# Performance work log

Measured on AMD Instinct MI355X. Metric: run time of the kernel, lower is better.

Reference implementation:

```python
import jax, jax.numpy as jnp
import numpy as np

B, S, DIM = 2, 2048, 768
HEADS, HEAD_DIM = 12, 64
WINDOW = 512
LEVELS, EXP = 4, 4
LR = 0.1
LN_EPS = 1e-5


def layernorm(x, g, b):
    m = jnp.mean(x, axis=-1, keepdims=True)
    v = jnp.mean(jnp.square(x - m), axis=-1, keepdims=True)
    return (x - m) * jax.lax.rsqrt(v + LN_EPS) * g + b


def setup_inputs() -> dict:
    key = jax.random.key(0)
    ks = jax.random.split(key, 12)
    D = DIM
    w = lambda k, shape: jax.random.normal(k, shape, jnp.float32) * 0.02
    return {
        "x": jax.random.normal(ks[0], (B, S, D), jnp.float32),
        # nn.MultiheadAttention params (packed qkv in_proj + out_proj)
        "in_proj_w": w(ks[1], (3 * D, D)),
        "in_proj_b": jnp.zeros((3 * D,), jnp.float32),
        "out_proj_w": w(ks[2], (D, D)),
        "out_proj_b": jnp.zeros((D,), jnp.float32),
        "ln_local_g": jnp.ones((D,), jnp.float32),
        "ln_local_b": jnp.zeros((D,), jnp.float32),
        # SelfModifyingTitans (delta-rule linear memory) params
        "t_wq": w(ks[3], (HEADS * HEAD_DIM, D)),
        "t_wk": w(ks[4], (HEADS * HEAD_DIM, D)),
        "t_wv": w(ks[5], (HEADS * HEAD_DIM, D)),
        "t_wo": w(ks[6], (D, HEADS * HEAD_DIM)),
        "ln_tit_g": jnp.ones((D,), jnp.float32),
        "ln_tit_b": jnp.zeros((D,), jnp.float32),
        # combine gate
        "gate_w": w(ks[7], (D, 2 * D)),
        "gate_b": jnp.zeros((D,), jnp.float32),
        # ContinuumMemorySystem: LEVELS stacked FFNs dim -> EXP*dim -> dim
        "cms_w1": w(ks[8], (LEVELS, EXP * D, D)),
        "cms_b1": jnp.zeros((LEVELS, EXP * D), jnp.float32),
        "cms_w2": w(ks[9], (LEVELS, D, EXP * D)),
        "cms_b2": jnp.zeros((LEVELS, D), jnp.float32),
        "ln_cms_g": jnp.ones((D,), jnp.float32),
        "ln_cms_b": jnp.zeros((D,), jnp.float32),
    }


def reference(x, in_proj_w, in_proj_b, out_proj_w, out_proj_b, ln_local_g,
              ln_local_b, t_wq, t_wk, t_wv, t_wo, ln_tit_g, ln_tit_b,
              gate_w, gate_b, cms_w1, cms_b1, cms_w2, cms_b2,
              ln_cms_g, ln_cms_b):
    Bq, Sq, D = x.shape
    H, dh = HEADS, D // HEADS

    # ---- causal sliding-window MHA (mask True = blocked in torch; here keep allowed) ----
    i = jnp.arange(Sq)[:, None]
    j = jnp.arange(Sq)[None, :]
    allowed = (j <= i) & (j > i - WINDOW)  # [S, S]

    qkv = x @ in_proj_w.T + in_proj_b  # [B,S,3D]
    q, k, v = jnp.split(qkv, 3, axis=-1)
    split_heads = lambda t: t.reshape(Bq, Sq, H, dh).transpose(0, 2, 1, 3)
    q, k, v = split_heads(q), split_heads(k), split_heads(v)
    scale = 1.0 / np.sqrt(dh).astype(np.float32)
    scores = jnp.einsum('bhqd,bhkd->bhqk', q * scale, k)
    scores = jnp.where(allowed, scores, jnp.finfo(scores.dtype).min)
    attn = jax.nn.softmax(scores, axis=-1)
    o = jnp.einsum('bhqk,bhkd->bhqd', attn, v)
    local_out = o.transpose(0, 2, 1, 3).reshape(Bq, Sq, D) @ out_proj_w.T + out_proj_b
    x_local = layernorm(x + local_out, ln_local_g, ln_local_b)

    # ---- SelfModifyingTitans: delta-rule recurrent associative memory ----
    tq = (x @ t_wq.T).reshape(Bq, Sq, HEADS, HEAD_DIM).transpose(1, 0, 2, 3)  # [S,B,H,dh]
    tk = (x @ t_wk.T).reshape(Bq, Sq, HEADS, HEAD_DIM).transpose(1, 0, 2, 3)
    tv = (x @ t_wv.T).reshape(Bq, Sq, HEADS, HEAD_DIM).transpose(1, 0, 2, 3)

    def step(M, qkv_t):
        qt, kt, vt = qkv_t  # each [B,H,dh]
        pred = jnp.einsum('bhde,bhd->bhe', M, kt)
        M = M + LR * jnp.einsum('bhd,bhe->bhde', kt, vt - pred)  # delta rule
        ot = jnp.einsum('bhde,bhd->bhe', M, qt)
        return M, ot

    M0 = jnp.zeros((Bq, HEADS, HEAD_DIM, HEAD_DIM), x.dtype)
    memory_state, os_seq = jax.lax.scan(step, M0, (tq, tk, tv))
    titans_out = os_seq.transpose(1, 0, 2, 3).reshape(Bq, Sq, HEADS * HEAD_DIM) @ t_wo.T
    x_global = layernorm(x + titans_out, ln_tit_g, ln_tit_b)

    # ---- gated combine ----
    gate = jax.nn.sigmoid(jnp.concatenate([x_local, x_global], axis=-1) @ gate_w.T + gate_b)
    xc = gate * x_local + (1.0 - gate) * x_global

    # ---- ContinuumMemorySystem: average of LEVELS FFNs ----
    h = jnp.einsum('bsd,lfd->blsf', xc, cms_w1) + cms_b1[None, :, None, :]
    h = jax.nn.gelu(h)
    cms = jnp.einsum('blsf,ldf->blsd', h, cms_w2) + cms_b2[None, :, None, :]
    cms_out = cms.mean(axis=1)

    out = layernorm(xc + cms_out, ln_cms_g, ln_cms_b)
    return out, memory_state
```

## Files before the change

### kernel.cpp

```cpp
#include <hip/hip_runtime.h>
#include <hip/hip_bf16.h>
#include <math.h>

typedef unsigned short u16;
typedef __attribute__((ext_vector_type(8))) short bf8v;
typedef __attribute__((ext_vector_type(4))) short bf4v;
typedef __attribute__((ext_vector_type(4))) float f4v;

__device__ __forceinline__ float bf2f(u16 h) {
    unsigned int u = ((unsigned int)h) << 16;
    float f;
    __builtin_memcpy(&f, &u, 4);
    return f;
}
__device__ __forceinline__ u16 f2bf(float f) {
    unsigned int u;
    __builtin_memcpy(&u, &f, 4);
    unsigned int r = (u + 0x7FFFu + ((u >> 16) & 1u)) >> 16;
    return (u16)r;
}
__device__ __forceinline__ float gelu_tanh(float x) {
    float x3 = x * x * x;
    float y = 0.7978845608028654f * (x + 0.044715f * x3);
    float e = __expf(2.f * y);
    float t = 1.f - 2.f / (e + 1.f);
    return 0.5f * x * (1.f + t);
}

#define SEQ 2048
#define DIMC 768
#define NHEAD 12
#define QKVC 2304
#define LRc 0.1f

__global__ __launch_bounds__(256) void cast_f2b_kernel(
    const float* __restrict__ src, u16* __restrict__ dst, int n)
{
    int i = (blockIdx.x * 256 + threadIdx.x) * 4;
    if (i + 3 < n) {
        float4 v = *(const float4*)(src + i);
        dst[i + 0] = f2bf(v.x);
        dst[i + 1] = f2bf(v.y);
        dst[i + 2] = f2bf(v.z);
        dst[i + 3] = f2bf(v.w);
    }
}

__global__ __launch_bounds__(256) void cast2_f2b_kernel(
    const float* __restrict__ s0, u16* __restrict__ d0,
    const float* __restrict__ s1, u16* __restrict__ d1, int n)
{
    const float* s = blockIdx.z ? s1 : s0;
    u16* d = blockIdx.z ? d1 : d0;
    int i = (blockIdx.x * 256 + threadIdx.x) * 4;
    if (i + 3 < n) {
        float4 v = *(const float4*)(s + i);
        d[i + 0] = f2bf(v.x);
        d[i + 1] = f2bf(v.y);
        d[i + 2] = f2bf(v.z);
        d[i + 3] = f2bf(v.w);
    }
}

__global__ __launch_bounds__(256) void cast_split_kernel(
    const float* __restrict__ src, u16* __restrict__ hi, u16* __restrict__ lo, int n)
{
    int i = (blockIdx.x * 256 + threadIdx.x) * 4;
    if (i + 3 < n) {
        float4 v = *(const float4*)(src + i);
        float vv[4] = {v.x, v.y, v.z, v.w};
        #pragma unroll
        for (int j = 0; j < 4; ++j) {
            u16 h = f2bf(vv[j]);
            hi[i + j] = h;
            lo[i + j] = f2bf(vv[j] - bf2f(h));
        }
    }
}

__device__ __forceinline__ void gemm128_body(
    const u16* __restrict__ A, const u16* __restrict__ W,
    const float* __restrict__ bias, u16* __restrict__ outb, float* __restrict__ outf,
    int N, int Kloop, int Kstride, int act, int mode, float oscale)
{
    __shared__ u16 As[128 * 32];
    __shared__ u16 Bs[128 * 32];
    const int tid  = threadIdx.x;
    const int lane = tid & 63;
    const int wv   = tid >> 6;
    const int r16  = lane & 15;
    const int quad = lane >> 4;
    const int mh   = (wv & 1) * 64;
    const int nh   = (wv >> 1) * 64;
    const int m_blk = blockIdx.x * 128;
    const int n_blk = blockIdx.y * 128;

    const int c0 = tid, c1 = tid + 256;
    const u16* Ag0 = A + (size_t)(m_blk + (c0 >> 2)) * Kstride + (c0 & 3) * 8;
    const u16* Ag1 = A + (size_t)(m_blk + (c1 >> 2)) * Kstride + (c1 & 3) * 8;
    const u16* Wg0 = W + (size_t)(n_blk + (c0 >> 2)) * Kstride + (c0 & 3) * 8;
    const u16* Wg1 = W + (size_t)(n_blk + (c1 >> 2)) * Kstride + (c1 & 3) * 8;
    u16* As0 = As + c0 * 8;
    u16* As1 = As + c1 * 8;
    u16* Bs0 = Bs + c0 * 8;
    u16* Bs1 = Bs + c1 * 8;

    f4v acc[4][4];
    #pragma unroll
    for (int i = 0; i < 4; ++i)
        #pragma unroll
        for (int j = 0; j < 4; ++j) acc[i][j] = (f4v){0.f, 0.f, 0.f, 0.f};

    bf8v av0 = *(const bf8v*)Ag0;
    bf8v av1 = *(const bf8v*)Ag1;
    bf8v bv0 = *(const bf8v*)Wg0;
    bf8v bv1 = *(const bf8v*)Wg1;
    for (int k0 = 0; k0 < Kloop; k0 += 32) {
        __syncthreads();
        *(bf8v*)As0 = av0;
        *(bf8v*)As1 = av1;
        *(bf8v*)Bs0 = bv0;
        *(bf8v*)Bs1 = bv1;
        __syncthreads();
        if (k0 + 32 < Kloop) {
            av0 = *(const bf8v*)(Ag0 + k0 + 32);
            av1 = *(const bf8v*)(Ag1 + k0 + 32);
            bv0 = *(const bf8v*)(Wg0 + k0 + 32);
            bv1 = *(const bf8v*)(Wg1 + k0 + 32);
        }
        bf8v af[4], bfj[4];
        #pragma unroll
        for (int i = 0; i < 4; ++i)
            af[i] = *(const bf8v*)(As + (mh + i * 16 + r16) * 32 + quad * 8);
        #pragma unroll
        for (int j = 0; j < 4; ++j)
            bfj[j] = *(const bf8v*)(Bs + (nh + j * 16 + r16) * 32 + quad * 8);
        #pragma unroll
        for (int i = 0; i < 4; ++i)
            #pragma unroll
            for (int j = 0; j < 4; ++j)
                acc[i][j] = __builtin_amdgcn_mfma_f32_16x16x32_bf16(af[i], bfj[j], acc[i][j], 0, 0, 0);
    }

    #pragma unroll
    for (int j = 0; j < 4; ++j) {
        int gn = n_blk + nh + j * 16 + r16;
        float bvv = bias ? bias[gn] : 0.f;
        #pragma unroll
        for (int i = 0; i < 4; ++i) {
            #pragma unroll
            for (int rr = 0; rr < 4; ++rr) {
                int gm = m_blk + mh + i * 16 + quad * 4 + rr;
                float v = acc[i][j][rr] + bvv;
                if (act == 1) v = gelu_tanh(v);
                else if (act == 2) v = 1.f / (1.f + __expf(-v));
                size_t oi = (size_t)gm * N + gn;
                if (mode == 0) outb[oi] = f2bf(v);
                else if (mode == 1) outf[oi] = oscale * v;
                else if (mode == 2) outf[oi] += oscale * v;
                else atomicAdd(outf + oi, oscale * v);
            }
        }
    }
}

__global__ __launch_bounds__(256) void gemm128_kernel(
    const u16* __restrict__ A, const u16* __restrict__ W,
    const float* __restrict__ bias, u16* __restrict__ outb, float* __restrict__ outf,
    int N, int K, int act, int mode, float oscale)
{
    gemm128_body(A, W, bias, outb, outf, N, K, K, act, mode, oscale);
}

__global__ __launch_bounds__(256) void gemm128_dual_kernel(
    const u16* __restrict__ A0, const u16* __restrict__ W0,
    const float* __restrict__ b0, u16* __restrict__ o0,
    const u16* __restrict__ A1, const u16* __restrict__ W1,
    const float* __restrict__ b1, u16* __restrict__ o1,
    int N, int K)
{
    if (blockIdx.z == 0) gemm128_body(A0, W0, b0, o0, nullptr, N, K, K, 0, 0, 0.f);
    else                 gemm128_body(A1, W1, b1, o1, nullptr, N, K, K, 0, 0, 0.f);
}

__global__ __launch_bounds__(256) void gemm128_ksplit_kernel(
    const u16* __restrict__ A, const u16* __restrict__ W,
    const float* __restrict__ bias, float* __restrict__ outf,
    int N, int Kstride, int KC, float oscale)
{
    const int z = blockIdx.z;
    gemm128_body(A + (size_t)z * KC, W + (size_t)z * KC, z == 0 ? bias : nullptr,
                 nullptr, outf, N, KC, Kstride, 0, 3, oscale);
}

__global__ __launch_bounds__(256) void gemm_split_kernel(
    const u16* __restrict__ Ahi, const u16* __restrict__ Alo,
    const u16* __restrict__ W0hi, const u16* __restrict__ W0lo, float* __restrict__ out0,
    const u16* __restrict__ W1hi, const u16* __restrict__ W1lo, float* __restrict__ out1,
    int M, int N, int K)
{
    const u16* Whi = blockIdx.z ? W1hi : W0hi;
    const u16* Wlo = blockIdx.z ? W1lo : W0lo;
    float* outf    = blockIdx.z ? out1 : out0;

    const int lane = threadIdx.x & 63;
    const int wv   = threadIdx.x >> 6;
    const int m0   = blockIdx.x * 64 + wv * 16;
    const int n0   = blockIdx.y * 64;
    const int r16  = lane & 15;
    const int quad = lane >> 4;

    const size_t arow = (size_t)(m0 + r16) * K + quad * 8;
    const size_t wrow = (size_t)(n0 + r16) * K + quad * 8;
    const size_t wstride = (size_t)16 * K;

    f4v acc[4];
    #pragma unroll
    for (int j = 0; j < 4; ++j) acc[j] = (f4v){0.f, 0.f, 0.f, 0.f};

    for (int k0 = 0; k0 < K; k0 += 32) {
        bf8v ah = *(const bf8v*)(Ahi + arow + k0);
        bf8v al = *(const bf8v*)(Alo + arow + k0);
        #pragma unroll
        for (int j = 0; j < 4; ++j) {
            bf8v bh = *(const bf8v*)(Whi + wrow + j * wstride + k0);
            bf8v bl = *(const bf8v*)(Wlo + wrow + j * wstride + k0);
            acc[j] = __builtin_amdgcn_mfma_f32_16x16x32_bf16(ah, bh, acc[j], 0, 0, 0);
            acc[j] = __builtin_amdgcn_mfma_f32_16x16x32_bf16(ah, bl, acc[j], 0, 0, 0);
            acc[j] = __builtin_amdgcn_mfma_f32_16x16x32_bf16(al, bh, acc[j], 0, 0, 0);
        }
    }

    #pragma unroll
    for (int j = 0; j < 4; ++j) {
        int gn = n0 + j * 16 + r16;
        #pragma unroll
        for (int rr = 0; rr < 4; ++rr) {
            int gm = m0 + quad * 4 + rr;
            outf[(size_t)gm * N + gn] = acc[j][rr];
        }
    }
}

#define NJ 527
#define NJP 548
__global__ __launch_bounds__(256) void attn_kernel(
    const u16* __restrict__ qkv, u16* __restrict__ outp)
{
    const int bh = blockIdx.y;
    const int b = bh / NHEAD, h = bh % NHEAD;
    const int q0 = blockIdx.x * 16;
    const int jbase = q0 - 511;
    const int tid = threadIdx.x;
    const int lane = tid & 63;
    const int wv = tid >> 6;
    const int r16 = lane & 15;
    const int quad = lane >> 4;

    __shared__ float ss[16][NJP];
    __shared__ float redbuf[16][17];
    __shared__ float rowmax[16];
    __shared__ float rowinv[16];

    const size_t qrow = (size_t)(b * SEQ + q0 + r16) * QKVC + h * 64 + quad * 8;
    bf8v qf0 = *(const bf8v*)(qkv + qrow);
    bf8v qf1 = *(const bf8v*)(qkv + qrow + 32);

    for (int jt = wv; jt < 33; jt += 4) {
        int js_l = jt * 16 + r16;
        int j = jbase + js_l;
        int jc = j & (SEQ - 1);
        const u16* kp = qkv + (size_t)(b * SEQ + jc) * QKVC + DIMC + h * 64 + quad * 8;
        bf8v kf0 = *(const bf8v*)kp;
        bf8v kf1 = *(const bf8v*)(kp + 32);
        f4v acc = (f4v){0.f, 0.f, 0.f, 0.f};
        acc = __builtin_amdgcn_mfma_f32_16x16x32_bf16(qf0, kf0, acc, 0, 0, 0);
        acc = __builtin_amdgcn_mfma_f32_16x16x32_bf16(qf1, kf1, acc, 0, 0, 0);
        if (js_l < NJ) {
            #pragma unroll
            for (int rr = 0; rr < 4; ++rr) {
                int row = quad * 4 + rr;
                bool ok = (j >= 0) && (js_l >= row) && (js_l <= row + 511);
                ss[row][js_l] = ok ? 0.125f * acc[rr] : -1e30f;
            }
        }
    }
    for (int t = tid; t < 16 * 17; t += 256)
        ss[t / 17][527 + t % 17] = 0.f;
    __syncthreads();

    {
        int r = tid >> 4, l16 = tid & 15;
        float mx = -1e30f;
        #pragma unroll 1
        for (int js = l16; js < NJ; js += 16) mx = fmaxf(mx, ss[r][js]);
        redbuf[r][l16] = mx;
        __syncthreads();
        if (l16 == 0) {
            float m = -1e30f;
            #pragma unroll
            for (int i = 0; i < 16; ++i) m = fmaxf(m, redbuf[r][i]);
            rowmax[r] = m;
        }
        __syncthreads();
        float rm = rowmax[r];
        float sm = 0.f;
        #pragma unroll 1
        for (int js = l16; js < NJ; js += 16) {
            float p = __expf(ss[r][js] - rm);
            ss[r][js] = p;
            sm += p;
        }
        redbuf[r][l16] = sm;
        __syncthreads();
        if (l16 == 0) {
            float s = 0.f;
            #pragma unroll
            for (int i = 0; i < 16; ++i) s += redbuf[r][i];
            rowinv[r] = 1.f / s;
        }
        __syncthreads();
    }

    {
        const int d0 = wv * 16;
        const u16* vp = qkv + (size_t)b * SEQ * QKVC + 2 * DIMC + h * 64 + d0 + r16;
        f4v oacc = (f4v){0.f, 0.f, 0.f, 0.f};
        for (int k0 = 0; k0 < 544; k0 += 32) {
            float4 p0 = *(const float4*)&ss[r16][k0 + quad * 8];
            float4 p1 = *(const float4*)&ss[r16][k0 + quad * 8 + 4];
            bf8v pa;
            pa[0] = (short)f2bf(p0.x); pa[1] = (short)f2bf(p0.y);
            pa[2] = (short)f2bf(p0.z); pa[3] = (short)f2bf(p0.w);
            pa[4] = (short)f2bf(p1.x); pa[5] = (short)f2bf(p1.y);
            pa[6] = (short)f2bf(p1.z); pa[7] = (short)f2bf(p1.w);
            bf8v vb;
            #pragma unroll
            for (int m = 0; m < 8; ++m) {
                int j = jbase + k0 + quad * 8 + m;
                int jc = j & (SEQ - 1);
                vb[m] = (short)vp[(size_t)jc * QKVC];
            }
            oacc = __builtin_amdgcn_mfma_f32_16x16x32_bf16(pa, vb, oacc, 0, 0, 0);
        }
        #pragma unroll
        for (int rr = 0; rr < 4; ++rr) {
            int row = quad * 4 + rr;
            size_t oi = (size_t)(b * SEQ + q0 + row) * DIMC + h * 64 + d0 + r16;
            outp[oi] = f2bf(oacc[rr] * rowinv[row]);
        }
    }
}

__global__ __launch_bounds__(256) void ln_res_kernel(
    const void* __restrict__ xv, int xf32, const void* __restrict__ yv, int yf32,
    const float* __restrict__ g, const float* __restrict__ be,
    u16* __restrict__ outb, float* __restrict__ outf, int ldout)
{
    const int row = blockIdx.x;
    const int t = threadIdx.x;
    const size_t base = (size_t)row * DIMC;
    float vv[3];
    float s = 0.f, s2 = 0.f;
    #pragma unroll
    for (int i = 0; i < 3; ++i) {
        int d = t + i * 256;
        float a = xf32 ? ((const float*)xv)[base + d] : bf2f(((const u16*)xv)[base + d]);
        float y = yf32 ? ((const float*)yv)[base + d] : bf2f(((const u16*)yv)[base + d]);
        float w = a + y;
        vv[i] = w;
        s += w;
        s2 += w * w;
    }
    #pragma unroll
    for (int o = 32; o > 0; o >>= 1) {
        s  += __shfl_down(s, o);
        s2 += __shfl_down(s2, o);
    }
    __shared__ float rs[4], rq[4], mb[2];
    if ((t & 63) == 0) { rs[t >> 6] = s; rq[t >> 6] = s2; }
    __syncthreads();
    if (t == 0) {
        float S1 = rs[0] + rs[1] + rs[2] + rs[3];
        float S2 = rq[0] + rq[1] + rq[2] + rq[3];
        float mean = S1 * (1.f / 768.f);
        float var = S2 * (1.f / 768.f) - mean * mean;
        mb[0] = mean;
        mb[1] = rsqrtf(var + 1e-5f);
    }
    __syncthreads();
    float mean = mb[0], rstd = mb[1];
    #pragma unroll
    for (int i = 0; i < 3; ++i) {
        int d = t + i * 256;
        float v = (vv[i] - mean) * rstd * g[d] + be[d];
        if (outb) outb[(size_t)row * ldout + d] = f2bf(v);
        else      outf[(size_t)row * ldout + d] = v;
    }
}

__global__ __launch_bounds__(256) void ln_res2_kernel(
    const float* __restrict__ x,
    const u16* __restrict__ y0, const float* __restrict__ g0, const float* __restrict__ b0,
    u16* __restrict__ o0,
    const u16* __restrict__ y1, const float* __restrict__ g1, const float* __restrict__ b1,
    u16* __restrict__ o1, int M)
{
    int row = blockIdx.x;
    const u16* y; const float* g; const float* be; u16* ob;
    if (row < M) { y = y0; g = g0; be = b0; ob = o0; }
    else { row -= M; y = y1; g = g1; be = b1; ob = o1; }
    const int t = threadIdx.x;
    const size_t base = (size_t)row * DIMC;
    float vv[3];
    float s = 0.f, s2 = 0.f;
    #pragma unroll
    for (int i = 0; i < 3; ++i) {
        int d = t + i * 256;
        float w = x[base + d] + bf2f(y[base + d]);
        vv[i] = w;
        s += w;
        s2 += w * w;
    }
    #pragma unroll
    for (int o = 32; o > 0; o >>= 1) {
        s  += __shfl_down(s, o);
        s2 += __shfl_down(s2, o);
    }
    __shared__ float rs[4], rq[4], mb[2];
    if ((t & 63) == 0) { rs[t >> 6] = s; rq[t >> 6] = s2; }
    __syncthreads();
    if (t == 0) {
        float S1 = rs[0] + rs[1] + rs[2] + rs[3];
        float S2 = rq[0] + rq[1] + rq[2] + rq[3];
        float mean = S1 * (1.f / 768.f);
        float var = S2 * (1.f / 768.f) - mean * mean;
        mb[0] = mean;
        mb[1] = rsqrtf(var + 1e-5f);
    }
    __syncthreads();
    float mean = mb[0], rstd = mb[1];
    #pragma unroll
    for (int i = 0; i < 3; ++i) {
        int d = t + i * 256;
        float v = (vv[i] - mean) * rstd * g[d] + be[d];
        ob[(size_t)row * 1536 + d] = f2bf(v);
    }
}

__global__ __launch_bounds__(64) void scanA_kernel(
    const u16* __restrict__ tq, const float* __restrict__ tk,
    float* __restrict__ Tm, float* __restrict__ Sm)
{
    const int bid = blockIdx.x;
    const int bh = bid >> 5, c = bid & 31;
    const int b = bh / NHEAD, h = bh % NHEAD;
    const int lane = threadIdx.x;

    __shared__ float Ks[64][68];
    __shared__ float As[64][68];
    __shared__ float Ts[64][68];
    __shared__ u16   Qs[64][72];

    const size_t rowb = (size_t)b * SEQ * DIMC + h * 64;
    const int rg = lane >> 4, c4 = (lane & 15) * 4;
    #pragma unroll 4
    for (int i = 0; i < 16; ++i) {
        int row = i * 4 + rg;
        size_t g = rowb + (size_t)(c * 64 + row) * DIMC + c4;
        *(float4*)&Ks[row][c4] = *(const float4*)(tk + g);
        *(bf4v*)&Qs[row][c4]   = *(const bf4v*)(tq + g);
    }
    __syncthreads();

    float4 kr4[16];
    #pragma unroll
    for (int d4 = 0; d4 < 16; ++d4) kr4[d4] = *(float4*)&Ks[lane][d4 * 4];

    for (int t = 0; t < 64; ++t) {
        float a = 0.f;
        #pragma unroll
        for (int d4 = 0; d4 < 16; ++d4) {
            float4 kt = *(float4*)&Ks[t][d4 * 4];
            a += kt.x * kr4[d4].x + kt.y * kr4[d4].y + kt.z * kr4[d4].z + kt.w * kr4[d4].w;
        }
        As[t][lane] = (lane < t) ? LRc * a : 0.f;
    }
    Ts[0][lane] = (lane == 0) ? 1.f : 0.f;
    for (int t = 1; t < 64; ++t) {
        float s = (lane == t) ? 1.f : 0.f;
        for (int tau = 0; tau < t; ++tau)
            s -= As[t][tau] * Ts[tau][lane];
        Ts[t][lane] = s;
    }
    for (int t = 0; t < 64; ++t) {
        float a = 0.f;
        #pragma unroll
        for (int d4 = 0; d4 < 16; ++d4) {
            bf4v qt = *(bf4v*)&Qs[t][d4 * 4];
            a += bf2f((u16)qt[0]) * kr4[d4].x + bf2f((u16)qt[1]) * kr4[d4].y
               + bf2f((u16)qt[2]) * kr4[d4].z + bf2f((u16)qt[3]) * kr4[d4].w;
        }
        As[t][lane] = (lane <= t) ? a : 0.f;
    }
    __syncthreads();
    float* Tg = Tm + (size_t)bid * 4096;
    float* Sg = Sm + (size_t)bid * 4096;
    #pragma unroll 4
    for (int i = 0; i < 16; ++i) {
        int row = i * 4 + rg;
        *(float4*)(Tg + row * 64 + c4) = *(float4*)&Ts[row][c4];
        *(float4*)(Sg + row * 64 + c4) = *(float4*)&As[row][c4];
    }
}

__global__ __launch_bounds__(256) void scanB_kernel(
    const u16* __restrict__ tq, const float* __restrict__ tk, const float* __restrict__ tv,
    const float* __restrict__ Tm, const float* __restrict__ Sm,
    u16* __restrict__ tito, float* __restrict__ mout)
{
    const int bid = blockIdx.x;
    const int bh = bid >> 2, eh = bid & 3;
    const int b = bh / NHEAD, h = bh % NHEAD;
    const int tid = threadIdx.x;
    const int tx = tid & 3;
    const int r  = tid >> 2;
    const int cc4 = tx * 4;
    const int e0 = eh * 16;

    __shared__ float Ms[64][20];
    __shared__ float Ys[64][20];
    __shared__ float Us[64][20];
    __shared__ float XK[64][68];
    __shared__ float XT[64][68];
    __shared__ float XS[64][68];
    __shared__ u16   Qt[64][72];

    const size_t rowb = (size_t)b * SEQ * DIMC + h * 64;

    for (int i = tid; i < 64 * 20; i += 256) (&Ms[0][0])[i] = 0.f;

    const int srow = tid & 63;
    const int scc  = (tid >> 6) * 16;

    for (int ch = 0; ch < 32; ++ch) {
        const size_t crow = rowb + (size_t)ch * 64 * DIMC;
        {
            const float* s = tk + crow + (size_t)srow * DIMC + scc;
            float4 a0 = *(const float4*)(s + 0), a1 = *(const float4*)(s + 4),
                   a2 = *(const float4*)(s + 8), a3 = *(const float4*)(s + 12);
            float av[16] = {a0.x, a0.y, a0.z, a0.w, a1.x, a1.y, a1.z, a1.w,
                            a2.x, a2.y, a2.z, a2.w, a3.x, a3.y, a3.z, a3.w};
            #pragma unroll
            for (int j = 0; j < 16; ++j) XK[scc + j][srow] = av[j];
            const u16* qg = tq + crow + (size_t)srow * DIMC + scc;
            bf8v q0 = *(const bf8v*)(qg), q1 = *(const bf8v*)(qg + 8);
            #pragma unroll
            for (int j = 0; j < 8; ++j) {
                Qt[scc + j][srow]     = (u16)q0[j];
                Qt[scc + 8 + j][srow] = (u16)q1[j];
            }
        }
        __syncthreads();

        const float* tsrc = Tm + ((size_t)(bh * 32 + ch)) * 4096 + (size_t)srow * 64 + scc;
        float4 t0 = *(const float4*)(tsrc + 0), t1 = *(const float4*)(tsrc + 4),
               t2 = *(const float4*)(tsrc + 8), t3 = *(const float4*)(tsrc + 12);
        float4 v0 = *(const float4*)(tv + crow + (size_t)r * DIMC + e0 + cc4);

        float p[4] = {0.f, 0.f, 0.f, 0.f};
        float oa[4] = {0.f, 0.f, 0.f, 0.f};
        #pragma unroll 4
        for (int k = 0; k < 64; ++k) {
            float a = XK[k][r];
            float q = bf2f(Qt[k][r]);
            float4 m = *(float4*)&Ms[k][cc4];
            p[0] += a * m.x; p[1] += a * m.y; p[2] += a * m.z; p[3] += a * m.w;
            oa[0] += q * m.x; oa[1] += q * m.y; oa[2] += q * m.z; oa[3] += q * m.w;
        }
        {
            float av[16] = {t0.x, t0.y, t0.z, t0.w, t1.x, t1.y, t1.z, t1.w,
                            t2.x, t2.y, t2.z, t2.w, t3.x, t3.y, t3.z, t3.w};
            #pragma unroll
            for (int j = 0; j < 16; ++j) XT[scc + j][srow] = av[j];
            Ys[r][cc4 + 0] = LRc * (v0.x - p[0]);
            Ys[r][cc4 + 1] = LRc * (v0.y - p[1]);
            Ys[r][cc4 + 2] = LRc * (v0.z - p[2]);
            Ys[r][cc4 + 3] = LRc * (v0.w - p[3]);
        }
        __syncthreads();

        const float* ssrc = Sm + ((size_t)(bh * 32 + ch)) * 4096 + (size_t)srow * 64 + scc;
        float4 s0 = *(const float4*)(ssrc + 0), s1 = *(const float4*)(ssrc + 4),
               s2 = *(const float4*)(ssrc + 8), s3 = *(const float4*)(ssrc + 12);

        float u[4] = {0.f, 0.f, 0.f, 0.f};
        #pragma unroll 4
        for (int k = 0; k < 64; ++k) {
            float a = XT[k][r];
            float4 bb = *(float4*)&Ys[k][cc4];
            u[0] += a * bb.x; u[1] += a * bb.y; u[2] += a * bb.z; u[3] += a * bb.w;
        }
        {
            float av[16] = {s0.x, s0.y, s0.z, s0.w, s1.x, s1.y, s1.z, s1.w,
                            s2.x, s2.y, s2.z, s2.w, s3.x, s3.y, s3.z, s3.w};
            #pragma unroll
            for (int j = 0; j < 16; ++j) XS[scc + j][srow] = av[j];
            #pragma unroll
            for (int j = 0; j < 4; ++j) Us[r][cc4 + j] = u[j];
        }
        __syncthreads();

        float m0[4];
        #pragma unroll
        for (int j = 0; j < 4; ++j) m0[j] = Ms[r][cc4 + j];
        #pragma unroll 4
        for (int k = 0; k < 64; ++k) {
            float sa = XS[k][r];
            float ka = XK[r][k];
            float4 uu = *(float4*)&Us[k][cc4];
            oa[0] += sa * uu.x; oa[1] += sa * uu.y; oa[2] += sa * uu.z; oa[3] += sa * uu.w;
            m0[0] += ka * uu.x; m0[1] += ka * uu.y; m0[2] += ka * uu.z; m0[3] += ka * uu.w;
        }
        #pragma unroll
        for (int j = 0; j < 4; ++j) Ms[r][cc4 + j] = m0[j];
        {
            u16* op = tito + crow + (size_t)r * DIMC + e0 + cc4;
            bf4v w;
            #pragma unroll
            for (int j = 0; j < 4; ++j) w[j] = (short)f2bf(oa[j]);
            *(bf4v*)op = w;
        }
        __syncthreads();
    }
    {
        float* mg = mout + (size_t)bh * 4096 + (size_t)r * 64 + e0 + cc4;
        *(float4*)mg = *(float4*)&Ms[r][cc4];
    }
}

__global__ __launch_bounds__(768) void combine_kernel(
    const u16* __restrict__ xlg, const u16* __restrict__ gate, u16* __restrict__ xc)
{
    const int row = blockIdx.x;
    const int t = threadIdx.x;
    float g = bf2f(gate[(size_t)row * DIMC + t]);
    float xl = bf2f(xlg[(size_t)row * 1536 + t]);
    float xg = bf2f(xlg[(size_t)row * 1536 + 768 + t]);
    xc[(size_t)row * DIMC + t] = f2bf(g * xl + (1.f - g) * xg);
}

extern "C" void kernel_launch(void* const* d_in, const int* in_sizes, int n_in,
                              void* d_out, int out_size, void* d_ws, size_t ws_size,
                              hipStream_t stream) {
    const float* x          = (const float*)d_in[0];
    const float* in_proj_w  = (const float*)d_in[1];
    const float* in_proj_b  = (const float*)d_in[2];
    const float* out_proj_w = (const float*)d_in[3];
    const float* out_proj_b = (const float*)d_in[4];
    const float* ln_local_g = (const float*)d_in[5];
    const float* ln_local_b = (const float*)d_in[6];
    const float* t_wq       = (const float*)d_in[7];
    const float* t_wk       = (const float*)d_in[8];
    const float* t_wv       = (const float*)d_in[9];
    const float* t_wo       = (const float*)d_in[10];
    const float* ln_tit_g   = (const float*)d_in[11];
    const float* ln_tit_b   = (const float*)d_in[12];
    const float* gate_w     = (const float*)d_in[13];
    const float* gate_b     = (const float*)d_in[14];
    const float* cms_w1     = (const float*)d_in[15];
    const float* cms_b1     = (const float*)d_in[16];
    const float* cms_w2     = (const float*)d_in[17];
    const float* cms_b2     = (const float*)d_in[18];
    const float* ln_cms_g   = (const float*)d_in[19];
    const float* ln_cms_b   = (const float*)d_in[20];

    const int Mrows = 2 * SEQ;

    u16* ws = (u16*)d_ws;
    u16*   qkv   = ws + 0;
    u16*   lout  = ws + 0;
    u16*   gout  = ws + 3145728;
    u16*   gact  = ws + 6291456;
    u16*   tq16  = ws + 9437184;
    u16*   wB    = ws + 9437184;
    u16*   wB2   = ws + 10027008;
    u16*   w_inp = ws + 12582912;
    float* tkf   = (float*)(ws + 12582912);
    u16*   W1S   = ws + 12582912;
    u16*   W2S   = ws + 14942208;
    float* tvf   = (float*)(ws + 18874368);
    u16*   w_tqb = ws + 25165824;
    u16*   tito  = ws + 25165824;
    u16*   w_hi  = ws + 28311552;
    u16*   w_lo  = ws + 28901376;
    u16*   w_hi2 = ws + 29491200;
    u16*   w_lo2 = ws + 30081024;
    u16*   attn_o= ws + 28311552;
    u16*   xc    = ws + 28311552;
    u16*   x_hi  = ws + 31457280;
    u16*   x_lo  = ws + 34603008;
    u16*   xlg   = ws + 31457280;
    u16*   h     = ws + 0;

    float* out32 = (float*)d_out;
    float* cmsacc = out32;
    float* mout  = out32 + (size_t)Mrows * DIMC;

    float* Tmat = (float*)(ws + 31457280);
    float* Smat = out32;

    auto cast = [&](const float* src, u16* dst, int n) {
        cast_f2b_kernel<<<(n + 1023) / 1024, 256, 0, stream>>>(src, dst, n);
    };
    auto gemm = [&](const u16* A, const u16* W, const float* bias, u16* ob, float* of,
                    int M, int N, int K, int act, int mode, float oscale) {
        gemm128_kernel<<<dim3(M / 128, N / 128), 256, 0, stream>>>(
            A, W, bias, ob, of, N, K, act, mode, oscale);
    };
    auto split = [&](const float* src, u16* hi, u16* lo, int n) {
        cast_split_kernel<<<(n + 1023) / 1024, 256, 0, stream>>>(src, hi, lo, n);
    };

    split(x, x_hi, x_lo, Mrows * DIMC);
    cast(in_proj_w, w_inp, QKVC * DIMC);
    gemm(x_hi, w_inp, in_proj_b, qkv, nullptr, Mrows, QKVC, DIMC, 0, 0, 0.f);
    split(t_wk, w_hi, w_lo, DIMC * DIMC);
    split(t_wv, w_hi2, w_lo2, DIMC * DIMC);
    gemm_split_kernel<<<dim3(Mrows / 64, DIMC / 64, 2), 256, 0, stream>>>(
        x_hi, x_lo, w_hi, w_lo, tkf, w_hi2, w_lo2, tvf, Mrows, DIMC, DIMC);
    cast(t_wq, w_tqb, DIMC * DIMC);
    gemm(x_hi, w_tqb, nullptr, tq16, nullptr, Mrows, DIMC, DIMC, 0, 0, 0.f);
    attn_kernel<<<dim3(SEQ / 16, 2 * NHEAD), 256, 0, stream>>>(qkv, attn_o);
    scanA_kernel<<<24 * 32, 64, 0, stream>>>(tq16, tkf, Tmat, Smat);
    scanB_kernel<<<24 * 4, 256, 0, stream>>>(tq16, tkf, tvf, Tmat, Smat, tito, mout);
    cast2_f2b_kernel<<<dim3((DIMC * DIMC + 1023) / 1024, 1, 2), 256, 0, stream>>>(
        out_proj_w, wB, t_wo, wB2, DIMC * DIMC);
    gemm128_dual_kernel<<<dim3(Mrows / 128, DIMC / 128, 2), 256, 0, stream>>>(
        attn_o, wB, out_proj_b, lout, tito, wB2, nullptr, gout, DIMC, DIMC);
    ln_res2_kernel<<<2 * Mrows, 256, 0, stream>>>(
        x, lout, ln_local_g, ln_local_b, xlg,
        gout, ln_tit_g, ln_tit_b, xlg + 768, Mrows);
    cast(gate_w, wB, DIMC * 2 * DIMC);
    gemm(xlg, wB, gate_b, gact, nullptr, Mrows, DIMC, 2 * DIMC, 2, 0, 0.f);
    combine_kernel<<<Mrows, 768, 0, stream>>>(xlg, gact, xc);
    hipMemsetAsync(cmsacc, 0, (size_t)Mrows * DIMC * sizeof(float), stream);
    for (int l = 0; l < 4; ++l) {
        cast2_f2b_kernel<<<dim3((2359296 + 1023) / 1024, 1, 2), 256, 0, stream>>>(
            cms_w1 + (size_t)l * 2359296, W1S, cms_w2 + (size_t)l * 2359296, W2S, 2359296);
        gemm(xc, W1S, cms_b1 + l * 3072, h, nullptr, Mrows, 3072, DIMC, 1, 0, 0.f);
        gemm128_ksplit_kernel<<<dim3(Mrows / 128, DIMC / 128, 4), 256, 0, stream>>>(
            h, W2S, cms_b2 + l * DIMC, cmsacc, DIMC, 3072, 768, 0.25f);
    }
    ln_res_kernel<<<Mrows, 256, 0, stream>>>(xc, 0, cmsacc, 1, ln_cms_g, ln_cms_b, nullptr, out32, DIMC);

    (void)in_sizes; (void)n_in; (void)out_size; (void)ws_size;
}
```

Baseline: 1.298 ms.

## Fuse sliding-window attention and delta-rule scan into one heterogeneous launch

Merges the attention kernel and the sequential scanB kernel into a single launch. The first 96 blocks run the serial delta-rule scan and the remaining 3072 blocks run attention, sharing one 75 KB shared buffer. This lets the long-latency, low-parallelism scan overlap with the attention work instead of running alone on few CUs. The cost is that attention blocks now reserve 75 KB of LDS instead of about 36 KB, which can reduce attention occupancy.

```diff
diff --git a/kernel.cpp b/kernel.cpp
--- a/kernel.cpp
+++ b/kernel.cpp
@@ -244,23 +244,26 @@
 
 #define NJ 527
 #define NJP 548
-__global__ __launch_bounds__(256) void attn_kernel(
-    const u16* __restrict__ qkv, u16* __restrict__ outp)
-{
-    const int bh = blockIdx.y;
+#define SCANB_BLOCKS 96
+#define FUSED_SMEM 76800
+
+__device__ void attn_dev(char* smem, int ab, const u16* __restrict__ qkv,
+                         u16* __restrict__ outp)
+{
+    float (*ss)[NJP]   = (float(*)[NJP])(smem);
+    float (*redbuf)[17]= (float(*)[17])(smem + 35072);
+    float* rowmax      = (float*)(smem + 36160);
+    float* rowinv      = (float*)(smem + 36224);
+
+    const int bh = ab >> 7;
     const int b = bh / NHEAD, h = bh % NHEAD;
-    const int q0 = blockIdx.x * 16;
+    const int q0 = (ab & 127) * 16;
     const int jbase = q0 - 511;
     const int tid = threadIdx.x;
     const int lane = tid & 63;
     const int wv = tid >> 6;
     const int r16 = lane & 15;
     const int quad = lane >> 4;
-
-    __shared__ float ss[16][NJP];
-    __shared__ float redbuf[16][17];
-    __shared__ float rowmax[16];
-    __shared__ float rowinv[16];
 
     const size_t qrow = (size_t)(b * SEQ + q0 + r16) * QKVC + h * 64 + quad * 8;
     bf8v qf0 = *(const bf8v*)(qkv + qrow);
@@ -352,6 +355,143 @@
     }
 }
 
+__device__ void scanB_dev(char* smem, int bid,
+    const u16* __restrict__ tq, const float* __restrict__ tk, const float* __restrict__ tv,
+    const float* __restrict__ Tm, const float* __restrict__ Sm,
+    u16* __restrict__ tito, float* __restrict__ mout)
+{
+    float (*Ms)[20] = (float(*)[20])(smem);
+    float (*Ys)[20] = (float(*)[20])(smem + 5120);
+    float (*Us)[20] = (float(*)[20])(smem + 10240);
+    float (*XK)[68] = (float(*)[68])(smem + 15360);
+    float (*XT)[68] = (float(*)[68])(smem + 32768);
+    float (*XS)[68] = (float(*)[68])(smem + 50176);
+    u16   (*Qt)[72] = (u16(*)[72])(smem + 67584);
+
+    const int bh = bid >> 2, eh = bid & 3;
+    const int b = bh / NHEAD, h = bh % NHEAD;
+    const int tid = threadIdx.x;
+    const int tx = tid & 3;
+    const int r  = tid >> 2;
+    const int cc4 = tx * 4;
+    const int e0 = eh * 16;
+
+    const size_t rowb = (size_t)b * SEQ * DIMC + h * 64;
+
+    for (int i = tid; i < 64 * 20; i += 256) (&Ms[0][0])[i] = 0.f;
+
+    const int srow = tid & 63;
+    const int scc  = (tid >> 6) * 16;
+
+    for (int ch = 0; ch < 32; ++ch) {
+        const size_t crow = rowb + (size_t)ch * 64 * DIMC;
+        {
+            const float* s = tk + crow + (size_t)srow * DIMC + scc;
+            float4 a0 = *(const float4*)(s + 0), a1 = *(const float4*)(s + 4),
+                   a2 = *(const float4*)(s + 8), a3 = *(const float4*)(s + 12);
+            float av[16] = {a0.x, a0.y, a0.z, a0.w, a1.x, a1.y, a1.z, a1.w,
+                            a2.x, a2.y, a2.z, a2.w, a3.x, a3.y, a3.z, a3.w};
+            #pragma unroll
+            for (int j = 0; j < 16; ++j) XK[scc + j][srow] = av[j];
+            const u16* qg = tq + crow + (size_t)srow * DIMC + scc;
+            bf8v q0 = *(const bf8v*)(qg), q1 = *(const bf8v*)(qg + 8);
+            #pragma unroll
+            for (int j = 0; j < 8; ++j) {
+                Qt[scc + j][srow]     = (u16)q0[j];
+                Qt[scc + 8 + j][srow] = (u16)q1[j];
+            }
+        }
+        __syncthreads();
+
+        const float* tsrc = Tm + ((size_t)(bh * 32 + ch)) * 4096 + (size_t)srow * 64 + scc;
+        float4 t0 = *(const float4*)(tsrc + 0), t1 = *(const float4*)(tsrc + 4),
+               t2 = *(const float4*)(tsrc + 8), t3 = *(const float4*)(tsrc + 12);
+        float4 v0 = *(const float4*)(tv + crow + (size_t)r * DIMC + e0 + cc4);
+
+        float p[4] = {0.f, 0.f, 0.f, 0.f};
+        float oa[4] = {0.f, 0.f, 0.f, 0.f};
+        #pragma unroll 4
+        for (int k = 0; k < 64; ++k) {
+            float a = XK[k][r];
+            float q = bf2f(Qt[k][r]);
+            float4 m = *(float4*)&Ms[k][cc4];
+            p[0] += a * m.x; p[1] += a * m.y; p[2] += a * m.z; p[3] += a * m.w;
+            oa[0] += q * m.x; oa[1] += q * m.y; oa[2] += q * m.z; oa[3] += q * m.w;
+        }
+        {
+            float av[16] = {t0.x, t0.y, t0.z, t0.w, t1.x, t1.y, t1.z, t1.w,
+                            t2.x, t2.y, t2.z, t2.w, t3.x, t3.y, t3.z, t3.w};
+            #pragma unroll
+            for (int j = 0; j < 16; ++j) XT[scc + j][srow] = av[j];
+            Ys[r][cc4 + 0] = LRc * (v0.x - p[0]);
+            Ys[r][cc4 + 1] = LRc * (v0.y - p[1]);
+            Ys[r][cc4 + 2] = LRc * (v0.z - p[2]);
+            Ys[r][cc4 + 3] = LRc * (v0.w - p[3]);
+        }
+        __syncthreads();
+
+        const float* ssrc = Sm + ((size_t)(bh * 32 + ch)) * 4096 + (size_t)srow * 64 + scc;
+        float4 s0 = *(const float4*)(ssrc + 0), s1 = *(const float4*)(ssrc + 4),
+               s2 = *(const float4*)(ssrc + 8), s3 = *(const float4*)(ssrc + 12);
+
+        float u[4] = {0.f, 0.f, 0.f, 0.f};
+        #pragma unroll 4
+        for (int k = 0; k < 64; ++k) {
+            float a = XT[k][r];
+            float4 bb = *(float4*)&Ys[k][cc4];
+            u[0] += a * bb.x; u[1] += a * bb.y; u[2] += a * bb.z; u[3] += a * bb.w;
+        }
+        {
+            float av[16] = {s0.x, s0.y, s0.z, s0.w, s1.x, s1.y, s1.z, s1.w,
+                            s2.x, s2.y, s2.z, s2.w, s3.x, s3.y, s3.z, s3.w};
+            #pragma unroll
+            for (int j = 0; j < 16; ++j) XS[scc + j][srow] = av[j];
+            #pragma unroll
+            for (int j = 0; j < 4; ++j) Us[r][cc4 + j] = u[j];
+        }
+        __syncthreads();
+
+        float m0[4];
+        #pragma unroll
+        for (int j = 0; j < 4; ++j) m0[j] = Ms[r][cc4 + j];
+        #pragma unroll 4
+        for (int k = 0; k < 64; ++k) {
+            float sa = XS[k][r];
+            float ka = XK[r][k];
+            float4 uu = *(float4*)&Us[k][cc4];
+            oa[0] += sa * uu.x; oa[1] += sa * uu.y; oa[2] += sa * uu.z; oa[3] += sa * uu.w;
+            m0[0] += ka * uu.x; m0[1] += ka * uu.y; m0[2] += ka * uu.z; m0[3] += ka * uu.w;
+        }
+        #pragma unroll
+        for (int j = 0; j < 4; ++j) Ms[r][cc4 + j] = m0[j];
+        {
+            u16* op = tito + crow + (size_t)r * DIMC + e0 + cc4;
+            bf4v w;
+            #pragma unroll
+            for (int j = 0; j < 4; ++j) w[j] = (short)f2bf(oa[j]);
+            *(bf4v*)op = w;
+        }
+        __syncthreads();
+    }
+    {
+        float* mg = mout + (size_t)bh * 4096 + (size_t)r * 64 + e0 + cc4;
+        *(float4*)mg = *(float4*)&Ms[r][cc4];
+    }
+}
+
+__global__ __launch_bounds__(256) void fused_attn_scan_kernel(
+    const u16* __restrict__ qkv, u16* __restrict__ outp,
+    const u16* __restrict__ tq, const float* __restrict__ tk, const float* __restrict__ tv,
+    const float* __restrict__ Tm, const float* __restrict__ Sm,
+    u16* __restrict__ tito, float* __restrict__ mout)
+{
+    __shared__ __align__(16) char smem[FUSED_SMEM];
+    if (blockIdx.x < SCANB_BLOCKS)
+        scanB_dev(smem, blockIdx.x, tq, tk, tv, Tm, Sm, tito, mout);
+    else
+        attn_dev(smem, blockIdx.x - SCANB_BLOCKS, qkv, outp);
+}
+
 __global__ __launch_bounds__(256) void ln_res_kernel(
     const void* __restrict__ xv, int xf32, const void* __restrict__ yv, int yf32,
     const float* __restrict__ g, const float* __restrict__ be,
@@ -511,131 +651,6 @@
         int row = i * 4 + rg;
         *(float4*)(Tg + row * 64 + c4) = *(float4*)&Ts[row][c4];
         *(float4*)(Sg + row * 64 + c4) = *(float4*)&As[row][c4];
-    }
-}
-
-__global__ __launch_bounds__(256) void scanB_kernel(
-    const u16* __restrict__ tq, const float* __restrict__ tk, const float* __restrict__ tv,
-    const float* __restrict__ Tm, const float* __restrict__ Sm,
-    u16* __restrict__ tito, float* __restrict__ mout)
-{
-    const int bid = blockIdx.x;
-    const int bh = bid >> 2, eh = bid & 3;
-    const int b = bh / NHEAD, h = bh % NHEAD;
-    const int tid = threadIdx.x;
-    const int tx = tid & 3;
-    const int r  = tid >> 2;
-    const int cc4 = tx * 4;
-    const int e0 = eh * 16;
-
-    __shared__ float Ms[64][20];
-    __shared__ float Ys[64][20];
-    __shared__ float Us[64][20];
-    __shared__ float XK[64][68];
-    __shared__ float XT[64][68];
-    __shared__ float XS[64][68];
-    __shared__ u16   Qt[64][72];
-
-    const size_t rowb = (size_t)b * SEQ * DIMC + h * 64;
-
-    for (int i = tid; i < 64 * 20; i += 256) (&Ms[0][0])[i] = 0.f;
-
-    const int srow = tid & 63;
-    const int scc  = (tid >> 6) * 16;
-
-    for (int ch = 0; ch < 32; ++ch) {
-        const size_t crow = rowb + (size_t)ch * 64 * DIMC;
-        {
-            const float* s = tk + crow + (size_t)srow * DIMC + scc;
-            float4 a0 = *(const float4*)(s + 0), a1 = *(const float4*)(s + 4),
-                   a2 = *(const float4*)(s + 8), a3 = *(const float4*)(s + 12);
-            float av[16] = {a0.x, a0.y, a0.z, a0.w, a1.x, a1.y, a1.z, a1.w,
-                            a2.x, a2.y, a2.z, a2.w, a3.x, a3.y, a3.z, a3.w};
-            #pragma unroll
-            for (int j = 0; j < 16; ++j) XK[scc + j][srow] = av[j];
-            const u16* qg = tq + crow + (size_t)srow * DIMC + scc;
-            bf8v q0 = *(const bf8v*)(qg), q1 = *(const bf8v*)(qg + 8);
-            #pragma unroll
-            for (int j = 0; j < 8; ++j) {
-                Qt[scc + j][srow]     = (u16)q0[j];
-                Qt[scc + 8 + j][srow] = (u16)q1[j];
-            }
-        }
-        __syncthreads();
-
-        const float* tsrc = Tm + ((size_t)(bh * 32 + ch)) * 4096 + (size_t)srow * 64 + scc;
-        float4 t0 = *(const float4*)(tsrc + 0), t1 = *(const float4*)(tsrc + 4),
-               t2 = *(const float4*)(tsrc + 8), t3 = *(const float4*)(tsrc + 12);
-        float4 v0 = *(const float4*)(tv + crow + (size_t)r * DIMC + e0 + cc4);
-
-        float p[4] = {0.f, 0.f, 0.f, 0.f};
-        float oa[4] = {0.f, 0.f, 0.f, 0.f};
-        #pragma unroll 4
-        for (int k = 0; k < 64; ++k) {
-            float a = XK[k][r];
-            float q = bf2f(Qt[k][r]);
-            float4 m = *(float4*)&Ms[k][cc4];
-            p[0] += a * m.x; p[1] += a * m.y; p[2] += a * m.z; p[3] += a * m.w;
-            oa[0] += q * m.x; oa[1] += q * m.y; oa[2] += q * m.z; oa[3] += q * m.w;
-        }
-        {
-            float av[16] = {t0.x, t0.y, t0.z, t0.w, t1.x, t1.y, t1.z, t1.w,
-                            t2.x, t2.y, t2.z, t2.w, t3.x, t3.y, t3.z, t3.w};
-            #pragma unroll
-            for (int j = 0; j < 16; ++j) XT[scc + j][srow] = av[j];
-            Ys[r][cc4 + 0] = LRc * (v0.x - p[0]);
-            Ys[r][cc4 + 1] = LRc * (v0.y - p[1]);
-            Ys[r][cc4 + 2] = LRc * (v0.z - p[2]);
-            Ys[r][cc4 + 3] = LRc * (v0.w - p[3]);
-        }
-        __syncthreads();
-
-        const float* ssrc = Sm + ((size_t)(bh * 32 + ch)) * 4096 + (size_t)srow * 64 + scc;
-        float4 s0 = *(const float4*)(ssrc + 0), s1 = *(const float4*)(ssrc + 4),
-               s2 = *(const float4*)(ssrc + 8), s3 = *(const float4*)(ssrc + 12);
-
-        float u[4] = {0.f, 0.f, 0.f, 0.f};
-        #pragma unroll 4
-        for (int k = 0; k < 64; ++k) {
-            float a = XT[k][r];
-            float4 bb = *(float4*)&Ys[k][cc4];
-            u[0] += a * bb.x; u[1] += a * bb.y; u[2] += a * bb.z; u[3] += a * bb.w;
-        }
-        {
-            float av[16] = {s0.x, s0.y, s0.z, s0.w, s1.x, s1.y, s1.z, s1.w,
-                            s2.x, s2.y, s2.z, s2.w, s3.x, s3.y, s3.z, s3.w};
-            #pragma unroll
-            for (int j = 0; j < 16; ++j) XS[scc + j][srow] = av[j];
-            #pragma unroll
-            for (int j = 0; j < 4; ++j) Us[r][cc4 + j] = u[j];
-        }
-        __syncthreads();
-
-        float m0[4];
-        #pragma unroll
-        for (int j = 0; j < 4; ++j) m0[j] = Ms[r][cc4 + j];
-        #pragma unroll 4
-        for (int k = 0; k < 64; ++k) {
-            float sa = XS[k][r];
-            float ka = XK[r][k];
-            float4 uu = *(float4*)&Us[k][cc4];
-            oa[0] += sa * uu.x; oa[1] += sa * uu.y; oa[2] += sa * uu.z; oa[3] += sa * uu.w;
-            m0[0] += ka * uu.x; m0[1] += ka * uu.y; m0[2] += ka * uu.z; m0[3] += ka * uu.w;
-        }
-        #pragma unroll
-        for (int j = 0; j < 4; ++j) Ms[r][cc4 + j] = m0[j];
-        {
-            u16* op = tito + crow + (size_t)r * DIMC + e0 + cc4;
-            bf4v w;
-            #pragma unroll
-            for (int j = 0; j < 4; ++j) w[j] = (short)f2bf(oa[j]);
-            *(bf4v*)op = w;
-        }
-        __syncthreads();
-    }
-    {
-        float* mg = mout + (size_t)bh * 4096 + (size_t)r * 64 + e0 + cc4;
-        *(float4*)mg = *(float4*)&Ms[r][cc4];
     }
 }
 
@@ -731,9 +746,9 @@
         x_hi, x_lo, w_hi, w_lo, tkf, w_hi2, w_lo2, tvf, Mrows, DIMC, DIMC);
     cast(t_wq, w_tqb, DIMC * DIMC);
     gemm(x_hi, w_tqb, nullptr, tq16, nullptr, Mrows, DIMC, DIMC, 0, 0, 0.f);
-    attn_kernel<<<dim3(SEQ / 16, 2 * NHEAD), 256, 0, stream>>>(qkv, attn_o);
     scanA_kernel<<<24 * 32, 64, 0, stream>>>(tq16, tkf, Tmat, Smat);
-    scanB_kernel<<<24 * 4, 256, 0, stream>>>(tq16, tkf, tvf, Tmat, Smat, tito, mout);
+    fused_attn_scan_kernel<<<SCANB_BLOCKS + 128 * 24, 256, 0, stream>>>(
+        qkv, attn_o, tq16, tkf, tvf, Tmat, Smat, tito, mout);
     cast2_f2b_kernel<<<dim3((DIMC * DIMC + 1023) / 1024, 1, 2), 256, 0, stream>>>(
         out_proj_w, wB, t_wo, wB2, DIMC * DIMC);
     gemm128_dual_kernel<<<dim3(Mrows / 128, DIMC / 128, 2), 256, 0, stream>>>(
```

Result: faster. 1.239 ms (-4.6%).
